# Kernel tuning notes

Measured on AMD Instinct MI355X. Metric: run time of the kernel, lower is better.

## Reference

```python
import jax, jax.numpy as jnp
import numpy as np

B, T, D, H = 2, 2048, 1024, 16
DK = D // H
NEG = -1e9  # stand-in for -inf; causal mask guarantees >=1 valid key per row


def setup_inputs() -> dict:
    key = jax.random.key(0)
    ks = jax.random.split(key, 9)
    s = 1.0 / np.sqrt(D)
    x = jax.random.normal(ks[0], (B, T, D), dtype=jnp.float32)
    mask = jnp.broadcast_to(jnp.tril(jnp.ones((T, T), dtype=jnp.int32))[None, None], (B, 1, T, T))
    params = {}
    for i, n in enumerate(['q', 'k', 'v', 'o']):
        params['W' + n] = jax.random.normal(ks[1 + 2 * i], (D, D), dtype=jnp.float32) * s
        params['b' + n] = jax.random.normal(ks[2 + 2 * i], (D,), dtype=jnp.float32) * s
    return dict(x=x, mask=mask, **params)


def reference(x, mask, Wq, bq, Wk, bk, Wv, bv, Wo, bo):
    Bx, Tx, Dx = x.shape
    # projections: [B,T,D] -> [B,H,T,DK]
    def split_heads(y):
        return y.reshape(Bx, Tx, H, DK).transpose(0, 2, 1, 3)
    Q = split_heads(x @ Wq + bq)
    K = split_heads(x @ Wk + bk)
    V = split_heads(x @ Wv + bv)
    scores = jnp.einsum('bhqd,bhkd->bhqk', Q, K) / jnp.sqrt(jnp.float32(DK))
    scores = jnp.where(mask == 0, NEG, scores)
    attn = jax.nn.softmax(scores, axis=-1)  # dropout is identity in eval / p=0
    out = jnp.einsum('bhqk,bhkd->bhqd', attn, V)
    out = out.transpose(0, 2, 1, 3).reshape(Bx, Tx, Dx)
    return out @ Wo + bo
```

## Files before the change

### kernel.cpp

```cpp
#include <hip/hip_runtime.h>
#include <hip/hip_bf16.h>

typedef __bf16 bf16;
typedef __attribute__((ext_vector_type(8))) __bf16 bf16x8;
typedef __attribute__((ext_vector_type(4))) __bf16 bf16x4;
typedef __attribute__((ext_vector_type(4))) float f32x4;

#define TSEQ 2048
#define DMODEL 1024
#define NHEAD 16
#define DKH 64
#define BATCH 2
#define NQKV 3072
#define PSTR 72

typedef __attribute__((address_space(1))) const void gv_t;
typedef __attribute__((address_space(3))) void sv_t;
__device__ __forceinline__ void gll16(const bf16* g, bf16* s) {
    __builtin_amdgcn_global_load_lds((gv_t*)g, (sv_t*)s, 16, 0, 0);
}
__device__ __forceinline__ void wait_vm0() {
    __builtin_amdgcn_s_waitcnt(0x0F70);
}

__global__ __launch_bounds__(256) void convert_bf16(
    const float* __restrict__ in, bf16* __restrict__ out)
{
    int i = (blockIdx.x * 256 + threadIdx.x) * 4;
    f32x4 v = *(const f32x4*)(in + i);
    bf16x4 o;
#pragma unroll
    for (int j = 0; j < 4; ++j) o[j] = (bf16)v[j];
    *(bf16x4*)(out + i) = o;
}

__global__ __launch_bounds__(256) void bias_concat(
    const float* __restrict__ bq, const float* __restrict__ bk,
    const float* __restrict__ bv, float* __restrict__ out)
{
    int i = blockIdx.x * 256 + threadIdx.x;
    float v = i < 1024 ? bq[i] : i < 2048 ? bk[i - 1024] : bv[i - 2048];
    out[i] = v;
}

__global__ __launch_bounds__(256) void transpose_w(
    const float* __restrict__ W0, const float* __restrict__ W1,
    const float* __restrict__ W2, const float* __restrict__ W3,
    bf16* __restrict__ WT)
{
    __shared__ float t[32][33];
    const float* W = blockIdx.z == 0 ? W0 : blockIdx.z == 1 ? W1
                   : blockIdx.z == 2 ? W2 : W3;
    bf16* T = WT + (size_t)blockIdx.z * DMODEL * DMODEL;
    int bx = blockIdx.x * 32, by = blockIdx.y * 32;
    int tx = threadIdx.x, ty = threadIdx.y;
#pragma unroll
    for (int i = 0; i < 4; ++i)
        t[ty + i * 8][tx] = W[(size_t)(by + ty + i * 8) * DMODEL + bx + tx];
    __syncthreads();
#pragma unroll
    for (int i = 0; i < 4; ++i)
        T[(size_t)(bx + ty + i * 8) * DMODEL + by + tx] = (bf16)t[tx][ty + i * 8];
}

__global__ __launch_bounds__(256) void transpose_v(
    const bf16* __restrict__ QKV, bf16* __restrict__ VT)
{
    __shared__ bf16 t[32][33];
    int b = blockIdx.z >> 4, h = blockIdx.z & 15;
    int t0 = blockIdx.x * 32, d0 = blockIdx.y * 32;
    int tx = threadIdx.x, ty = threadIdx.y;
#pragma unroll
    for (int i = 0; i < 4; ++i)
        t[ty + i * 8][tx] =
            QKV[(size_t)(b * TSEQ + t0 + ty + i * 8) * NQKV + 2048 + h * DKH + d0 + tx];
    __syncthreads();
#pragma unroll
    for (int i = 0; i < 4; ++i)
        VT[((size_t)(b * NHEAD + h) * DKH + d0 + ty + i * 8) * TSEQ + t0 + tx] =
            t[tx][ty + i * 8];
}

template <typename OutT, int NW_N>
__global__ __launch_bounds__(256) void gemm_bias_kernel(
    const bf16* __restrict__ A, const bf16* __restrict__ BT,
    const float* __restrict__ bias, OutT* __restrict__ C, int ldc)
{
    constexpr int BN    = NW_N * 64;
    constexpr int MW    = 4 / NW_N;
    constexpr int WROWS = 128 / MW;
    constexpr int FM    = WROWS / 16;
    constexpr int ASZ   = 128 * 32;
    constexpr int BSZ   = BN * 32;
    constexpr int BNP   = BN + 4;
    constexpr int EPI   = sizeof(OutT) == 2 ? 128 * BN : 64 * BNP * 2;
    constexpr int SMEM  = (2 * ASZ + 2 * BSZ) > EPI ? (2 * ASZ + 2 * BSZ) : EPI;
    __shared__ bf16 smem[SMEM];
    bf16* As0 = smem;
    bf16* Bs0 = smem + 2 * ASZ;

    const int tid = threadIdx.x;
    const int ln = tid & 63, wave = tid >> 6;
    const int wm = NW_N == 2 ? (wave >> 1) : wave;
    const int wn = NW_N == 2 ? (wave & 1) : 0;
    const int lr = ln & 15, quad = ln >> 4;
    const int m0 = blockIdx.y * 128, n0 = blockIdx.x * BN;

    f32x4 acc[FM][4] = {};

    const int grow = ln >> 2;
    const int gcol = (ln & 3) * 8;
    const bf16* Ag = A + (size_t)(m0 + wave * 32 + grow) * DMODEL + gcol;
    const bf16* Bg = BT + (size_t)(n0 + (NW_N == 2 ? wave * 32 : wave * 16) + grow) * DMODEL + gcol;

    auto stage = [&](int buf, int kk) {
        bf16* AsW = As0 + buf * ASZ + wave * 1024;
        gll16(Ag + kk, AsW);
        gll16(Ag + (size_t)16 * DMODEL + kk, AsW + 512);
        if constexpr (NW_N == 2) {
            bf16* BsW = Bs0 + buf * BSZ + wave * 1024;
            gll16(Bg + kk, BsW);
            gll16(Bg + (size_t)16 * DMODEL + kk, BsW + 512);
        } else {
            gll16(Bg + kk, Bs0 + buf * BSZ + wave * 512);
        }
    };

    constexpr int NT = DMODEL / 32;
    stage(0, 0);
    wait_vm0();
    __syncthreads();
    for (int kt = 0; kt < NT; ++kt) {
        if (kt + 1 < NT) stage((kt + 1) & 1, (kt + 1) * 32);
        const bf16* AsB = As0 + (kt & 1) * ASZ;
        const bf16* BsB = Bs0 + (kt & 1) * BSZ;
        bf16x8 af[FM], bfr[4];
#pragma unroll
        for (int i = 0; i < FM; ++i)
            af[i] = *(const bf16x8*)(AsB + (wm * WROWS + i * 16 + lr) * 32 + quad * 8);
#pragma unroll
        for (int j = 0; j < 4; ++j)
            bfr[j] = *(const bf16x8*)(BsB + (wn * 64 + j * 16 + lr) * 32 + quad * 8);
#pragma unroll
        for (int i = 0; i < FM; ++i)
#pragma unroll
            for (int j = 0; j < 4; ++j)
                acc[i][j] = __builtin_amdgcn_mfma_f32_16x16x32_bf16(
                    af[i], bfr[j], acc[i][j], 0, 0, 0);
        wait_vm0();
        __syncthreads();
    }

    if constexpr (sizeof(OutT) == 2) {
        bf16* Cs = smem;
#pragma unroll
        for (int j = 0; j < 4; ++j) {
            int nl = wn * 64 + j * 16 + lr;
            float bv = bias[n0 + nl];
#pragma unroll
            for (int i = 0; i < FM; ++i) {
                int ml = wm * WROWS + i * 16 + quad * 4;
#pragma unroll
                for (int r = 0; r < 4; ++r)
                    Cs[(ml + r) * BN + nl] = (bf16)(acc[i][j][r] + bv);
            }
        }
        __syncthreads();
        constexpr int LPR = BN / 8;
        constexpr int RPP = 256 / LPR;
        const int rr = tid / LPR, cc = (tid % LPR) * 8;
#pragma unroll
        for (int p = 0; p < 128 / RPP; ++p) {
            int row = p * RPP + rr;
            *(bf16x8*)(C + (size_t)(m0 + row) * ldc + n0 + cc) =
                *(const bf16x8*)(Cs + row * BN + cc);
        }
    } else {
        float* Cf = (float*)smem;
#pragma unroll
        for (int half = 0; half < 2; ++half) {
            if (((wm * WROWS) >> 6) == half) {
#pragma unroll
                for (int j = 0; j < 4; ++j) {
                    int nl = wn * 64 + j * 16 + lr;
                    float bv = bias[n0 + nl];
#pragma unroll
                    for (int i = 0; i < FM; ++i) {
                        int ml = wm * WROWS + i * 16 + quad * 4 - half * 64;
#pragma unroll
                        for (int r = 0; r < 4; ++r)
                            Cf[(ml + r) * BNP + nl] = acc[i][j][r] + bv;
                    }
                }
            }
            __syncthreads();
            constexpr int LPR = BN / 4;
            constexpr int RPP = 256 / LPR;
            const int rr = tid / LPR, cc = (tid % LPR) * 4;
#pragma unroll
            for (int p = 0; p < 64 / RPP; ++p) {
                int row = p * RPP + rr;
                *(f32x4*)(C + (size_t)(m0 + half * 64 + row) * ldc + n0 + cc) =
                    *(const f32x4*)(Cf + row * BNP + cc);
            }
            __syncthreads();
        }
    }
}

template <bool MASK>
__device__ __forceinline__ void attn_chunk(
    int kc, int q0w, int lr, int quad,
    const bf16* __restrict__ KsB, const bf16* __restrict__ VsB,
    bf16* __restrict__ Pw,
    const bf16x8 qb[2], f32x4 oacc[4], float& lrow)
{
    const int sw = lr & 7;
    bf16x8 kb[4][2];
#pragma unroll
    for (int kt = 0; kt < 4; ++kt)
#pragma unroll
        for (int kk = 0; kk < 2; ++kk)
            kb[kt][kk] = *(const bf16x8*)(KsB + (kt * 16 + lr) * 64 +
                                          (((kk * 4 + quad) ^ sw) * 8));
    f32x4 st[4] = {};
#pragma unroll
    for (int kt = 0; kt < 4; ++kt)
#pragma unroll
        for (int kk = 0; kk < 2; ++kk)
            st[kt] = __builtin_amdgcn_mfma_f32_16x16x32_bf16(
                kb[kt][kk], qb[kk], st[kt], 0, 0, 0);

    const float scale2 = 0.18033688f;
    const int q = q0w + lr;
    float rs = 0.f;
#pragma unroll
    for (int kt = 0; kt < 4; ++kt) {
        bf16x4 p4;
#pragma unroll
        for (int r = 0; r < 4; ++r) {
            float p = exp2f(fmaf(st[kt][r], scale2, -24.0f));
            if (MASK && (kc + kt * 16 + quad * 4 + r > q)) p = 0.f;
            rs += p;
            p4[r] = (bf16)p;
        }
        *(bf16x4*)(Pw + lr * PSTR + kt * 16 + quad * 4) = p4;
    }
    rs += __shfl_xor(rs, 16);
    rs += __shfl_xor(rs, 32);
    lrow += rs;

#pragma unroll
    for (int kk = 0; kk < 2; ++kk) {
        bf16x8 pa = *(const bf16x8*)(Pw + lr * PSTR + kk * 32 + quad * 8);
#pragma unroll
        for (int dt = 0; dt < 4; ++dt) {
            bf16x8 vb = *(const bf16x8*)(VsB + (dt * 16 + lr) * 64 +
                                         (((kk * 4 + quad) ^ sw) * 8));
            oacc[dt] = __builtin_amdgcn_mfma_f32_16x16x32_bf16(
                pa, vb, oacc[dt], 0, 0, 0);
        }
    }
}

__global__ __launch_bounds__(512) void flash_attn(
    const bf16* __restrict__ QKV, const bf16* __restrict__ VT,
    bf16* __restrict__ O)
{
    __shared__ bf16 Ks[2][64 * 64];
    __shared__ bf16 Vs[2][64 * 64];
    __shared__ bf16 Pl[8][16 * PSTR];
    const int tid = threadIdx.x;
    const int ln = tid & 63, w = tid >> 6;
    const int lr = ln & 15, quad = ln >> 4;
    const int h = blockIdx.y, b = blockIdx.z;

    int xb = blockIdx.x;
    if ((h ^ b) & 1) xb = (TSEQ / 128 - 1) - xb;
    const int q0 = xb * 128;
    const int q0w = q0 + w * 16;
    bf16* Pw = Pl[w];

    const bf16* Qb = QKV + (size_t)b * TSEQ * NQKV + h * DKH;
    const bf16* Kb = Qb + 1024;
    const bf16* VTb = VT + (size_t)(b * NHEAD + h) * DKH * TSEQ;

    const int srow = (w & 3) * 16 + (ln >> 3);
    const int scol = ((ln & 7) ^ ((ln >> 3) & 7)) * 8;
    const bool stK = (w < 4);

    auto stage = [&](int buf, int kc) {
        if (stK) {
            const bf16* g = Kb + (size_t)(kc + srow) * NQKV + scol;
            bf16* s = &Ks[buf][(w & 3) * 16 * 64];
#pragma unroll
            for (int l = 0; l < 2; ++l)
                gll16(g + (size_t)(l * 8) * NQKV, s + l * 8 * 64);
        } else {
            const bf16* g = VTb + (size_t)srow * TSEQ + kc + scol;
            bf16* s = &Vs[buf][(w & 3) * 16 * 64];
#pragma unroll
            for (int l = 0; l < 2; ++l)
                gll16(g + (size_t)(l * 8) * TSEQ, s + l * 8 * 64);
        }
    };

    bf16x8 qb[2];
#pragma unroll
    for (int kk = 0; kk < 2; ++kk)
        qb[kk] = *(const bf16x8*)(Qb + (size_t)(q0w + lr) * NQKV +
                                  kk * 32 + quad * 8);

    f32x4 oacc[4] = {};
    float lrow = 0.f;

    const int nch = (q0 + 128) >> 6;
    stage(0, 0);
    wait_vm0();
    __syncthreads();
    for (int c = 0; c < nch; ++c) {
        if (c + 1 < nch) stage((c + 1) & 1, (c + 1) * 64);
        const int kc = c * 64;
        if (kc <= q0w + 15) {
            if (kc + 63 <= q0w)
                attn_chunk<false>(kc, q0w, lr, quad, Ks[c & 1], Vs[c & 1], Pw,
                                  qb, oacc, lrow);
            else
                attn_chunk<true>(kc, q0w, lr, quad, Ks[c & 1], Vs[c & 1], Pw,
                                 qb, oacc, lrow);
        }
        wait_vm0();
        __syncthreads();
    }

#pragma unroll
    for (int r = 0; r < 4; ++r) {
        float inv = 1.0f / __shfl(lrow, quad * 4 + r);
        int row = q0w + quad * 4 + r;
#pragma unroll
        for (int dt = 0; dt < 4; ++dt)
            O[(size_t)(b * TSEQ + row) * DMODEL + h * DKH + dt * 16 + lr] =
                (bf16)(oacc[dt][r] * inv);
    }
}

extern "C" void kernel_launch(void* const* d_in, const int* in_sizes, int n_in,
                              void* d_out, int out_size, void* d_ws, size_t ws_size,
                              hipStream_t stream)
{
    const float* x  = (const float*)d_in[0];
    const float* Wq = (const float*)d_in[2];
    const float* bq = (const float*)d_in[3];
    const float* Wk = (const float*)d_in[4];
    const float* bk = (const float*)d_in[5];
    const float* Wv = (const float*)d_in[6];
    const float* bv = (const float*)d_in[7];
    const float* Wo = (const float*)d_in[8];
    const float* bo = (const float*)d_in[9];

    char* ws = (char*)d_ws;
    bf16* xb   = (bf16*)(ws);
    bf16* QKV  = (bf16*)(ws + (8u  << 20));
    bf16* VT   = (bf16*)(ws + (32u << 20));
    bf16* O    = (bf16*)(ws + (40u << 20));
    bf16* WT   = (bf16*)(ws + (48u << 20));
    float* wsBias = (float*)VT;

    const int NX = BATCH * TSEQ * DMODEL;
    convert_bf16<<<NX / (256 * 4), 256, 0, stream>>>(x, xb);

    dim3 tb(32, 8);
    transpose_w<<<dim3(32, 32, 4), tb, 0, stream>>>(Wq, Wk, Wv, Wo, WT);
    bias_concat<<<NQKV / 256, 256, 0, stream>>>(bq, bk, bv, wsBias);

    gemm_bias_kernel<bf16, 2><<<dim3(NQKV / 128, 32), 256, 0, stream>>>(
        xb, WT, wsBias, QKV, NQKV);

    transpose_v<<<dim3(TSEQ / 32, DKH / 32, BATCH * NHEAD), tb, 0, stream>>>(QKV, VT);

    flash_attn<<<dim3(TSEQ / 128, NHEAD, BATCH), 512, 0, stream>>>(QKV, VT, O);

    gemm_bias_kernel<float, 1><<<dim3(DMODEL / 64, 32), 256, 0, stream>>>(
        O, WT + 3u * (1u << 20), bo, (float*)d_out, DMODEL);
}
```

Before: 218.0 us.

## Fuse prep kernels and shrink flash-attention blocks to 64 queries

Three preprocessing kernels (x conversion, weight transpose, bias concat) are merged into one launch to cut launch overhead. The flash attention kernel now uses 256-thread blocks covering 64 query rows instead of 512 threads covering 128. This doubles the grid, lowers LDS per block and makes every chunk except the last one unmasked. The P scratch buffer also switches from a padded stride to an XOR-swizzled layout to avoid LDS bank conflicts, which saves shared memory. K/V tiles are now staged to LDS once per 64 query rows instead of once per 128, so global-to-LDS traffic for K/V goes up.

```diff
diff --git a/kernel.cpp b/kernel.cpp
--- a/kernel.cpp
+++ b/kernel.cpp
@@ -12,7 +12,6 @@
 #define DKH 64
 #define BATCH 2
 #define NQKV 3072
-#define PSTR 72
 
 typedef __attribute__((address_space(1))) const void gv_t;
 typedef __attribute__((address_space(3))) void sv_t;
@@ -23,44 +22,49 @@
     __builtin_amdgcn_s_waitcnt(0x0F70);
 }
 
-__global__ __launch_bounds__(256) void convert_bf16(
-    const float* __restrict__ in, bf16* __restrict__ out)
-{
-    int i = (blockIdx.x * 256 + threadIdx.x) * 4;
-    f32x4 v = *(const f32x4*)(in + i);
-    bf16x4 o;
-#pragma unroll
-    for (int j = 0; j < 4; ++j) o[j] = (bf16)v[j];
-    *(bf16x4*)(out + i) = o;
-}
-
-__global__ __launch_bounds__(256) void bias_concat(
+#define PREP_CONV 4096
+#define PREP_TW   4096
+#define PREP_GRID (PREP_CONV + PREP_TW + 12)
+__global__ __launch_bounds__(256) void prep(
+    const float* __restrict__ x,
+    const float* __restrict__ Wq, const float* __restrict__ Wk,
+    const float* __restrict__ Wv, const float* __restrict__ Wo,
     const float* __restrict__ bq, const float* __restrict__ bk,
-    const float* __restrict__ bv, float* __restrict__ out)
-{
-    int i = blockIdx.x * 256 + threadIdx.x;
+    const float* __restrict__ bv,
+    bf16* __restrict__ xb, bf16* __restrict__ WT, float* __restrict__ biasO)
+{
+    __shared__ float t[32][33];
+    int bid = blockIdx.x;
+    const int tid = threadIdx.x;
+    if (bid < PREP_CONV) {
+        int i = (bid * 256 + tid) * 4;
+        f32x4 v = *(const f32x4*)(x + i);
+        bf16x4 o;
+#pragma unroll
+        for (int j = 0; j < 4; ++j) o[j] = (bf16)v[j];
+        *(bf16x4*)(xb + i) = o;
+        return;
+    }
+    bid -= PREP_CONV;
+    if (bid < PREP_TW) {
+        int z = bid >> 10;
+        int by = ((bid >> 5) & 31) * 32, bx = (bid & 31) * 32;
+        const float* W = z == 0 ? Wq : z == 1 ? Wk : z == 2 ? Wv : Wo;
+        bf16* T = WT + (size_t)z * DMODEL * DMODEL;
+        int tx = tid & 31, ty = tid >> 5;
+#pragma unroll
+        for (int i = 0; i < 4; ++i)
+            t[ty + i * 8][tx] = W[(size_t)(by + ty + i * 8) * DMODEL + bx + tx];
+        __syncthreads();
+#pragma unroll
+        for (int i = 0; i < 4; ++i)
+            T[(size_t)(bx + ty + i * 8) * DMODEL + by + tx] = (bf16)t[tx][ty + i * 8];
+        return;
+    }
+    bid -= PREP_TW;
+    int i = bid * 256 + tid;
     float v = i < 1024 ? bq[i] : i < 2048 ? bk[i - 1024] : bv[i - 2048];
-    out[i] = v;
-}
-
-__global__ __launch_bounds__(256) void transpose_w(
-    const float* __restrict__ W0, const float* __restrict__ W1,
-    const float* __restrict__ W2, const float* __restrict__ W3,
-    bf16* __restrict__ WT)
-{
-    __shared__ float t[32][33];
-    const float* W = blockIdx.z == 0 ? W0 : blockIdx.z == 1 ? W1
-                   : blockIdx.z == 2 ? W2 : W3;
-    bf16* T = WT + (size_t)blockIdx.z * DMODEL * DMODEL;
-    int bx = blockIdx.x * 32, by = blockIdx.y * 32;
-    int tx = threadIdx.x, ty = threadIdx.y;
-#pragma unroll
-    for (int i = 0; i < 4; ++i)
-        t[ty + i * 8][tx] = W[(size_t)(by + ty + i * 8) * DMODEL + bx + tx];
-    __syncthreads();
-#pragma unroll
-    for (int i = 0; i < 4; ++i)
-        T[(size_t)(bx + ty + i * 8) * DMODEL + by + tx] = (bf16)t[tx][ty + i * 8];
+    biasO[i] = v;
 }
 
 __global__ __launch_bounds__(256) void transpose_v(
@@ -244,7 +248,8 @@
             rs += p;
             p4[r] = (bf16)p;
         }
-        *(bf16x4*)(Pw + lr * PSTR + kt * 16 + quad * 4) = p4;
+        *(bf16x4*)(Pw + lr * 64 + (((kt * 2 + (quad >> 1)) ^ sw) * 8) +
+                   (quad & 1) * 4) = p4;
     }
     rs += __shfl_xor(rs, 16);
     rs += __shfl_xor(rs, 32);
@@ -252,7 +257,7 @@
 
 #pragma unroll
     for (int kk = 0; kk < 2; ++kk) {
-        bf16x8 pa = *(const bf16x8*)(Pw + lr * PSTR + kk * 32 + quad * 8);
+        bf16x8 pa = *(const bf16x8*)(Pw + lr * 64 + (((kk * 4 + quad) ^ sw) * 8));
 #pragma unroll
         for (int dt = 0; dt < 4; ++dt) {
             bf16x8 vb = *(const bf16x8*)(VsB + (dt * 16 + lr) * 64 +
@@ -263,21 +268,21 @@
     }
 }
 
-__global__ __launch_bounds__(512) void flash_attn(
+__global__ __launch_bounds__(256, 4) void flash_attn(
     const bf16* __restrict__ QKV, const bf16* __restrict__ VT,
     bf16* __restrict__ O)
 {
     __shared__ bf16 Ks[2][64 * 64];
     __shared__ bf16 Vs[2][64 * 64];
-    __shared__ bf16 Pl[8][16 * PSTR];
+    __shared__ bf16 Pl[4][16 * 64];
     const int tid = threadIdx.x;
     const int ln = tid & 63, w = tid >> 6;
     const int lr = ln & 15, quad = ln >> 4;
     const int h = blockIdx.y, b = blockIdx.z;
 
     int xb = blockIdx.x;
-    if ((h ^ b) & 1) xb = (TSEQ / 128 - 1) - xb;
-    const int q0 = xb * 128;
+    if ((h ^ b) & 1) xb = (TSEQ / 64 - 1) - xb;
+    const int q0 = xb * 64;
     const int q0w = q0 + w * 16;
     bf16* Pw = Pl[w];
 
@@ -285,22 +290,22 @@
     const bf16* Kb = Qb + 1024;
     const bf16* VTb = VT + (size_t)(b * NHEAD + h) * DKH * TSEQ;
 
-    const int srow = (w & 3) * 16 + (ln >> 3);
+    const int srow = (w & 1) * 32 + (ln >> 3);
     const int scol = ((ln & 7) ^ ((ln >> 3) & 7)) * 8;
-    const bool stK = (w < 4);
+    const bool stK = (w < 2);
 
     auto stage = [&](int buf, int kc) {
         if (stK) {
             const bf16* g = Kb + (size_t)(kc + srow) * NQKV + scol;
-            bf16* s = &Ks[buf][(w & 3) * 16 * 64];
-#pragma unroll
-            for (int l = 0; l < 2; ++l)
+            bf16* s = &Ks[buf][(w & 1) * 32 * 64];
+#pragma unroll
+            for (int l = 0; l < 4; ++l)
                 gll16(g + (size_t)(l * 8) * NQKV, s + l * 8 * 64);
         } else {
             const bf16* g = VTb + (size_t)srow * TSEQ + kc + scol;
-            bf16* s = &Vs[buf][(w & 3) * 16 * 64];
-#pragma unroll
-            for (int l = 0; l < 2; ++l)
+            bf16* s = &Vs[buf][(w & 1) * 32 * 64];
+#pragma unroll
+            for (int l = 0; l < 4; ++l)
                 gll16(g + (size_t)(l * 8) * TSEQ, s + l * 8 * 64);
         }
     };
@@ -314,21 +319,19 @@
     f32x4 oacc[4] = {};
     float lrow = 0.f;
 
-    const int nch = (q0 + 128) >> 6;
+    const int nch = xb + 1;
     stage(0, 0);
     wait_vm0();
     __syncthreads();
     for (int c = 0; c < nch; ++c) {
         if (c + 1 < nch) stage((c + 1) & 1, (c + 1) * 64);
         const int kc = c * 64;
-        if (kc <= q0w + 15) {
-            if (kc + 63 <= q0w)
-                attn_chunk<false>(kc, q0w, lr, quad, Ks[c & 1], Vs[c & 1], Pw,
-                                  qb, oacc, lrow);
-            else
-                attn_chunk<true>(kc, q0w, lr, quad, Ks[c & 1], Vs[c & 1], Pw,
-                                 qb, oacc, lrow);
-        }
+        if (c + 1 < nch)
+            attn_chunk<false>(kc, q0w, lr, quad, Ks[c & 1], Vs[c & 1], Pw,
+                              qb, oacc, lrow);
+        else
+            attn_chunk<true>(kc, q0w, lr, quad, Ks[c & 1], Vs[c & 1], Pw,
+                             qb, oacc, lrow);
         wait_vm0();
         __syncthreads();
     }
@@ -366,19 +369,16 @@
     bf16* WT   = (bf16*)(ws + (48u << 20));
     float* wsBias = (float*)VT;
 
-    const int NX = BATCH * TSEQ * DMODEL;
-    convert_bf16<<<NX / (256 * 4), 256, 0, stream>>>(x, xb);
-
-    dim3 tb(32, 8);
-    transpose_w<<<dim3(32, 32, 4), tb, 0, stream>>>(Wq, Wk, Wv, Wo, WT);
-    bias_concat<<<NQKV / 256, 256, 0, stream>>>(bq, bk, bv, wsBias);
+    prep<<<PREP_GRID, 256, 0, stream>>>(x, Wq, Wk, Wv, Wo, bq, bk, bv,
+                                        xb, WT, wsBias);
 
     gemm_bias_kernel<bf16, 2><<<dim3(NQKV / 128, 32), 256, 0, stream>>>(
         xb, WT, wsBias, QKV, NQKV);
 
+    dim3 tb(32, 8);
     transpose_v<<<dim3(TSEQ / 32, DKH / 32, BATCH * NHEAD), tb, 0, stream>>>(QKV, VT);
 
-    flash_attn<<<dim3(TSEQ / 128, NHEAD, BATCH), 512, 0, stream>>>(QKV, VT, O);
+    flash_attn<<<dim3(TSEQ / 64, NHEAD, BATCH), 256, 0, stream>>>(QKV, VT, O);
 
     gemm_bias_kernel<float, 1><<<dim3(DMODEL / 64, 32), 256, 0, stream>>>(
         O, WT + 3u * (1u << 20), bo, (float*)d_out, DMODEL);
```

New measurement: 212.5 us. -2.5%, faster.
